# Optimization experiments

Measured on AMD Instinct MI355X. Metric: run time of the kernel, lower is better.

Reference implementation:

```python
import jax, jax.numpy as jnp
import numpy as np

B, S, D_IN, D_OUT = 4, 2048, 1024, 1024

def setup_inputs() -> dict:
    key = jax.random.key(0)
    ks = jax.random.split(key, 6)
    s = 1.0 / np.sqrt(D_IN)
    return {
        "inputs": jax.random.normal(ks[0], (B, S, D_IN), dtype=jnp.float32),
        "Wq": jax.random.normal(ks[1], (D_IN, D_OUT), dtype=jnp.float32) * s,
        "Wk": jax.random.normal(ks[2], (D_IN, D_OUT), dtype=jnp.float32) * s,
        "Wv": jax.random.normal(ks[3], (D_IN, D_OUT), dtype=jnp.float32) * s,
        "Wo": jax.random.normal(ks[4], (D_OUT, D_OUT), dtype=jnp.float32) * (1.0 / np.sqrt(D_OUT)),
        "bo": jax.random.normal(ks[5], (D_OUT,), dtype=jnp.float32) * 0.01,
    }

def reference(inputs, Wq, Wk, Wv, Wo, bo):
    # QKV projections (no bias, matching qkv_bias=False)
    q = inputs @ Wq  # [B,S,D]
    k = inputs @ Wk
    v = inputs @ Wv
    # naive full attention: scores [B,S,S]
    scores = jnp.einsum('bqd,bkd->bqk', q, k) / jnp.sqrt(jnp.asarray(k.shape[-1], q.dtype))
    attn = jax.nn.softmax(scores, axis=-1)
    out = jnp.einsum('bqk,bkd->bqd', attn, v)
    return out @ Wo + bo
```

## Files before the change

kernel.cpp:

```cpp
#include <hip/hip_runtime.h>
#include <hip/hip_bf16.h>
#include <cstdint>

typedef __attribute__((ext_vector_type(8))) __bf16 bf16x8;
typedef __attribute__((ext_vector_type(4))) float  f32x4;

__device__ __forceinline__ unsigned short f2bf(float x) {
    union { float f; unsigned u; } v; v.f = x;
    unsigned r = v.u + 0x7fffu + ((v.u >> 16) & 1u);
    return (unsigned short)(r >> 16);
}
__device__ __forceinline__ unsigned pack2bf(float a, float b) {
    return (unsigned)f2bf(a) | ((unsigned)f2bf(b) << 16);
}

__device__ __forceinline__ void gld_lds16(const unsigned short* g, unsigned short* l) {
    __builtin_amdgcn_global_load_lds(
        (const __attribute__((address_space(1))) unsigned int*)g,
        (__attribute__((address_space(3))) unsigned int*)l,
        16, 0, 0);
}

__global__ void cvt_kernel(const float* __restrict__ in, unsigned short* __restrict__ out, int n4) {
    int i = blockIdx.x * blockDim.x + threadIdx.x;
    if (i < n4) {
        float4 f = ((const float4*)in)[i];
        ushort4 o;
        o.x = f2bf(f.x); o.y = f2bf(f.y); o.z = f2bf(f.z); o.w = f2bf(f.w);
        ((ushort4*)out)[i] = o;
    }
}

__global__ void wpack_kernel(const float* __restrict__ W, unsigned short* __restrict__ out) {
    int tid  = threadIdx.x;
    int lane = tid & 63;
    int chunk = blockIdx.x * 4 + (tid >> 6);
    int nt = chunk >> 5, k32 = chunk & 31;
    int r = lane & 15, q = lane >> 4;
    const float* src = W + (size_t)(k32*32 + q*8) * 1024 + nt*16 + r;
    unsigned o[4];
#pragma unroll
    for (int i = 0; i < 4; i++)
        o[i] = pack2bf(src[(size_t)(2*i) * 1024], src[(size_t)(2*i+1) * 1024]);
    *(uint4*)(out + (size_t)chunk * 512 + lane * 8) = make_uint4(o[0], o[1], o[2], o[3]);
}

__global__ void softmax_kernel(unsigned short* __restrict__ S) {
    const size_t row = blockIdx.x;
    unsigned short* p = S + row * 2048;
    const int tid = threadIdx.x;
    const int wave = tid >> 6, lane = tid & 63;

    uint4 raw = ((const uint4*)p)[tid];
    unsigned u[4] = {raw.x, raw.y, raw.z, raw.w};
    float x[8];
#pragma unroll
    for (int i = 0; i < 4; i++) {
        x[2*i]   = __uint_as_float(u[i] << 16);
        x[2*i+1] = __uint_as_float(u[i] & 0xffff0000u);
    }
    float m = x[0];
#pragma unroll
    for (int i = 1; i < 8; i++) m = fmaxf(m, x[i]);
#pragma unroll
    for (int off = 32; off >= 1; off >>= 1) m = fmaxf(m, __shfl_xor(m, off, 64));
    __shared__ float sm[4], ss[4];
    if (lane == 0) sm[wave] = m;
    __syncthreads();
    m = fmaxf(fmaxf(sm[0], sm[1]), fmaxf(sm[2], sm[3]));

    float e[8], s = 0.f;
#pragma unroll
    for (int i = 0; i < 8; i++) { e[i] = __expf(x[i] - m); s += e[i]; }
#pragma unroll
    for (int off = 32; off >= 1; off >>= 1) s += __shfl_xor(s, off, 64);
    if (lane == 0) ss[wave] = s;
    __syncthreads();
    s = ss[0] + ss[1] + ss[2] + ss[3];
    float inv = 1.0f / s;

    unsigned o[4];
#pragma unroll
    for (int i = 0; i < 4; i++)
        o[i] = pack2bf(e[2*i] * inv, e[2*i+1] * inv);
    ((uint4*)p)[tid] = make_uint4(o[0], o[1], o[2], o[3]);
}

template<int EPI>
__global__ __launch_bounds__(512, 2)
void gemm8p(const unsigned short* __restrict__ A, const unsigned short* __restrict__ Bpk,
            void* __restrict__ C, unsigned short* __restrict__ Ck, unsigned short* __restrict__ Cv,
            int lda, int ldc, int KS, int ns, float scale,
            long long sA, long long sB, long long sC)
{
    __shared__ __align__(16) char smem[131072];

    const int tid  = threadIdx.x;
    const int lane = tid & 63;
    const int wave = tid >> 6;
    const int bz = blockIdx.z;
    A   += (size_t)bz * sA;
    Bpk += (size_t)bz * sB;

    const int gx = gridDim.x;
    int lin = blockIdx.y * gx + blockIdx.x;
    int cpx = (gx * gridDim.y) >> 3;
    int swz = (lin & 7) * cpx + (lin >> 3);
    const int bm = (swz / gx) * 256;
    const int bn = (swz % gx) * 256;

    const int wm = (wave & 1) * 128;
    const int wn = (wave >> 1) * 64;
    const int ln15 = lane & 15;
    const int quad = lane >> 4;
    const int fko = (quad ^ ((ln15 >> 1) & 3)) * 8;

    const int srow = tid >> 2;
    const int scol = ((tid & 3) ^ ((tid >> 3) & 3)) * 8;
    const unsigned short* paU = A + (size_t)(bm + srow) * lda + scol;
    const unsigned short* paL = A + (size_t)(bm + 128 + srow) * lda + scol;
    const unsigned short* pb0 = Bpk + (size_t)((bn >> 4) + (tid >> 6)) * KS * 512 + lane * 8;
    const long long pbstep = (long long)8 * KS * 512;

    f32x4 acc[8][4];
#pragma unroll
    for (int i = 0; i < 8; i++)
#pragma unroll
        for (int j = 0; j < 4; j++) acc[i][j] = (f32x4){0.f, 0.f, 0.f, 0.f};

    auto stageA = [&](int buf, int t, int k) {
        char* d = smem + buf * 32768 + k * 16384 + tid * 16;
        const unsigned short* s = paU + t * 64 + k * 32;
        gld_lds16(s, (unsigned short*)d);
        gld_lds16(paL + t * 64 + k * 32, (unsigned short*)(d + 8192));
    };
    auto stageB = [&](int buf, int t, int k) {
        char* d = smem + 65536 + buf * 32768 + k * 16384 + (tid >> 6) * 1024 + lane * 16;
        const unsigned short* s = pb0 + (size_t)(2 * t + k) * 512;
        gld_lds16(s, (unsigned short*)d);
        gld_lds16(s + pbstep, (unsigned short*)(d + 8192));
    };
    auto dsread = [&](int buf, int k, int mh, bf16x8* af, bf16x8* bfr) {
        const unsigned short* Ar = (const unsigned short*)(smem + buf * 32768 + k * 16384);
        const unsigned short* Br = (const unsigned short*)(smem + 65536 + buf * 32768 + k * 16384);
#pragma unroll
        for (int i = 0; i < 4; i++)
            af[i] = *(const bf16x8*)&Ar[(wm + mh * 64 + i * 16 + ln15) * 32 + fko];
#pragma unroll
        for (int j = 0; j < 4; j++)
            bfr[j] = *(const bf16x8*)&Br[((wn >> 4) + j) * 512 + lane * 8];
    };
    auto mfma16 = [&](int mh, const bf16x8* af, const bf16x8* bfr) {
        __builtin_amdgcn_s_setprio(1);
#pragma unroll
        for (int i = 0; i < 4; i++)
#pragma unroll
            for (int j = 0; j < 4; j++)
                acc[mh * 4 + i][j] = __builtin_amdgcn_mfma_f32_16x16x32_bf16(
                    af[i], bfr[j], acc[mh * 4 + i][j], 0, 0, 0);
        __builtin_amdgcn_s_setprio(0);
    };

#define SB    __builtin_amdgcn_sched_barrier(0)
#define BAR   __builtin_amdgcn_s_barrier()
#define LGKM0 asm volatile("s_waitcnt lgkmcnt(0)" ::: "memory")
#define VM4   asm volatile("s_waitcnt vmcnt(4)" ::: "memory")

    stageB(0, 0, 0); stageA(0, 0, 0); stageB(0, 0, 1); stageA(0, 0, 1); SB;
    VM4; SB; BAR; SB;

    bf16x8 af[4], bfr[4];
    for (int t = 0; t < ns; ++t) {
        const int buf = t & 1, nb = buf ^ 1;
        const int tn = (t + 1 < ns) ? t + 1 : 0;
        dsread(buf, 0, 0, af, bfr); SB; stageB(nb, tn, 0); SB; BAR; SB;
        LGKM0; SB; mfma16(0, af, bfr); SB; BAR; SB;
        dsread(buf, 0, 1, af, bfr); SB; stageA(nb, tn, 0); SB; BAR; SB;
        LGKM0; SB; mfma16(1, af, bfr); SB; VM4; SB; BAR; SB;
        dsread(buf, 1, 0, af, bfr); SB; stageB(nb, tn, 1); SB; BAR; SB;
        LGKM0; SB; mfma16(0, af, bfr); SB; BAR; SB;
        dsread(buf, 1, 1, af, bfr); SB; stageA(nb, tn, 1); SB; BAR; SB;
        LGKM0; SB; mfma16(1, af, bfr); SB; VM4; SB; BAR; SB;
    }
#undef SB
#undef BAR
#undef LGKM0
#undef VM4

    if (EPI == 1) {
        __syncthreads();
        float* ep = (float*)(smem + wave * 4352);
        unsigned short* Co = (unsigned short*)C + (size_t)bz * sC;
#pragma unroll
        for (int i = 0; i < 8; i++) {
#pragma unroll
            for (int j = 0; j < 4; j++)
#pragma unroll
                for (int r = 0; r < 4; r++)
                    ep[(quad*4 + r) * 68 + j*16 + ln15] = acc[i][j][r] * scale;
            __builtin_amdgcn_s_waitcnt(0);
#pragma unroll
            for (int pp = 0; pp < 2; pp++) {
                int lrow = pp*8 + (lane >> 3);
                int col0 = (lane & 7) * 8;
                float4 lo = *(const float4*)&ep[lrow * 68 + col0];
                float4 hi = *(const float4*)&ep[lrow * 68 + col0 + 4];
                uint4 o;
                o.x = pack2bf(lo.x, lo.y); o.y = pack2bf(lo.z, lo.w);
                o.z = pack2bf(hi.x, hi.y); o.w = pack2bf(hi.z, hi.w);
                *(uint4*)&Co[(size_t)(bm + wm + i*16 + lrow) * ldc + bn + wn + col0] = o;
            }
            __builtin_amdgcn_s_waitcnt(0);
        }
    } else {
        __syncthreads();
        float* ep = (float*)(smem + wave * 8704);
        const int region = bn >> 10;
#pragma unroll
        for (int g = 0; g < 4; g++) {
#pragma unroll
            for (int ii = 0; ii < 2; ii++) {
                int i = g*2 + ii;
#pragma unroll
                for (int j = 0; j < 4; j++)
#pragma unroll
                    for (int r = 0; r < 4; r++)
                        ep[(ii*16 + quad*4 + r) * 68 + j*16 + ln15] = acc[i][j][r] * scale;
            }
            __builtin_amdgcn_s_waitcnt(0);
            const int mrow0 = bm + wm + g*32;
            if (region == 0) {
                unsigned short* Q = (unsigned short*)C;
#pragma unroll
                for (int pp = 0; pp < 4; pp++) {
                    int lrow = pp*8 + (lane >> 3);
                    int col0 = (lane & 7) * 8;
                    float4 lo = *(const float4*)&ep[lrow * 68 + col0];
                    float4 hi = *(const float4*)&ep[lrow * 68 + col0 + 4];
                    uint4 o;
                    o.x = pack2bf(lo.x, lo.y); o.y = pack2bf(lo.z, lo.w);
                    o.z = pack2bf(hi.x, hi.y); o.w = pack2bf(hi.z, hi.w);
                    *(uint4*)&Q[(size_t)(mrow0 + lrow) * ldc + bn + wn + col0] = o;
                }
            } else if (region == 1) {
#pragma unroll
                for (int mt = 0; mt < 2; mt++)
#pragma unroll
                    for (int c = 0; c < 2; c++) {
                        float4 f0 = *(const float4*)&ep[(mt*16 + ln15) * 68 + c*32 + quad*8];
                        float4 f1 = *(const float4*)&ep[(mt*16 + ln15) * 68 + c*32 + quad*8 + 4];
                        uint4 o;
                        o.x = pack2bf(f0.x, f0.y); o.y = pack2bf(f0.z, f0.w);
                        o.z = pack2bf(f1.x, f1.y); o.w = pack2bf(f1.z, f1.w);
                        int cid = ((mrow0 + mt*16) >> 4) * 32 + ((bn - 1024 + wn + c*32) >> 5);
                        *(uint4*)(Ck + (size_t)cid * 512 + lane * 8) = o;
                    }
            } else {
                int s32 = mrow0 >> 5;
#pragma unroll
                for (int dt = 0; dt < 4; dt++) {
                    float v[8];
#pragma unroll
                    for (int e = 0; e < 8; e++)
                        v[e] = ep[(quad*8 + e) * 68 + dt*16 + ln15];
                    uint4 o;
                    o.x = pack2bf(v[0], v[1]); o.y = pack2bf(v[2], v[3]);
                    o.z = pack2bf(v[4], v[5]); o.w = pack2bf(v[6], v[7]);
                    int cid = (((bn - 2048 + wn) >> 4) + dt) * 256 + s32;
                    *(uint4*)(Cv + (size_t)cid * 512 + lane * 8) = o;
                }
            }
            __builtin_amdgcn_s_waitcnt(0);
        }
    }
}

template<int EPI>
__global__ __launch_bounds__(512, 2)
void gemm_pk(const unsigned short* __restrict__ A, const unsigned short* __restrict__ Bpk,
             void* __restrict__ C, unsigned short* __restrict__ Ck, unsigned short* __restrict__ Cv,
             const float* __restrict__ bias,
             int lda, int ldc, int KS, int ns, float scale,
             long long sA, long long sB, long long sC)
{
    __shared__ __align__(16) char smem[98304];

    const int tid  = threadIdx.x;
    const int lane = tid & 63;
    const int wave = tid >> 6;
    const int bz = blockIdx.z;
    A   += (size_t)bz * sA;
    Bpk += (size_t)bz * sB;

    const int gx = gridDim.x;
    int lin = blockIdx.y * gx + blockIdx.x;
    int cpx = (gx * gridDim.y) >> 3;
    int swz = (lin & 7) * cpx + (lin >> 3);
    const int bm = (swz / gx) * 256;
    const int bn = (swz % gx) * 128;

    const int srow = tid >> 2;
    const int scol = ((tid & 3) ^ ((tid >> 3) & 3)) * 8;
    const unsigned short* pa0 = A + (size_t)(bm + srow) * lda + scol;
    const unsigned short* pa1 = pa0 + 32;
    const unsigned short* pa2 = A + (size_t)(bm + 128 + srow) * lda + scol;
    const unsigned short* pa3 = pa2 + 32;

    const int wm = (wave & 3) * 64;
    const int wn = (wave >> 2) * 64;
    const int ln15 = lane & 15;
    const int quad = lane >> 4;
    const int fko = (quad ^ ((ln15 >> 1) & 3)) * 8;
    const int rbase = (wm >> 7) * 4096 + (wm & 127) * 32;
    const int ldsoff = tid * 16;

    const unsigned short* pb[4];
#pragma unroll
    for (int j = 0; j < 4; j++)
        pb[j] = Bpk + (size_t)(((bn + wn + j*16) >> 4) * KS) * 512 + lane * 8;

    f32x4 acc[4][4];
#pragma unroll
    for (int i = 0; i < 4; i++)
#pragma unroll
        for (int j = 0; j < 4; j++) acc[i][j] = (f32x4){0.f, 0.f, 0.f, 0.f};

    auto dma = [&](int buf) {
        char* base = smem + buf * 32768;
        gld_lds16(pa0, (unsigned short*)(base + ldsoff));
        gld_lds16(pa2, (unsigned short*)(base + 8192  + ldsoff));
        gld_lds16(pa1, (unsigned short*)(base + 16384 + ldsoff));
        gld_lds16(pa3, (unsigned short*)(base + 24576 + ldsoff));
        pa0 += 64; pa1 += 64; pa2 += 64; pa3 += 64;
    };
    auto loadB = [&](bf16x8* br) {
#pragma unroll
        for (int j = 0; j < 4; j++) {
            br[j]     = *(const bf16x8*)(pb[j]);
            br[4 + j] = *(const bf16x8*)(pb[j] + 512);
            pb[j] += 1024;
        }
    };
    auto phase = [&](const unsigned short* As, int t, const bf16x8* br) {
        bf16x8 af[4];
#pragma unroll
        for (int i = 0; i < 4; i++)
            af[i] = *(const bf16x8*)&As[t*8192 + rbase + i*512 + ln15*32 + fko];
        __builtin_amdgcn_s_setprio(1);
#pragma unroll
        for (int i = 0; i < 4; i++)
#pragma unroll
            for (int j = 0; j < 4; j++)
                acc[i][j] = __builtin_amdgcn_mfma_f32_16x16x32_bf16(
                    af[i], br[t*4 + j], acc[i][j], 0, 0, 0);
        __builtin_amdgcn_s_setprio(0);
    };

#define SB __builtin_amdgcn_sched_barrier(0)
    bf16x8 b0[8], b1[8];
    SB; dma(0); SB; loadB(b0); SB; dma(1); SB;

    int p = 0;
    for (int it = 0; it < ns; it += 2) {
        const unsigned short* As0 = (const unsigned short*)(smem + p * 32768);
        int p1 = p + 1; if (p1 >= 3) p1 -= 3;
        int q0 = p + 2; if (q0 >= 3) q0 -= 3;
        const unsigned short* As1 = (const unsigned short*)(smem + p1 * 32768);
        const bool more = (it + 2 < ns);

        asm volatile("s_waitcnt vmcnt(12)" ::: "memory");
        SB; __builtin_amdgcn_s_barrier(); SB;
        loadB(b1); SB;
        phase(As0, 0, b0);
        __builtin_amdgcn_s_barrier(); SB;
        if (more) { dma(q0); SB; }
        phase(As0, 1, b0);

        if (more) { asm volatile("s_waitcnt vmcnt(12)" ::: "memory"); }
        else      { asm volatile("s_waitcnt vmcnt(8)"  ::: "memory"); }
        SB; __builtin_amdgcn_s_barrier(); SB;
        if (more) { loadB(b0); SB; }
        phase(As1, 0, b1);
        __builtin_amdgcn_s_barrier(); SB;
        if (it + 3 < ns) { dma(p); SB; }
        phase(As1, 1, b1);

        p = q0;
    }
#undef SB

    if (EPI == 0) {
        float bval[4];
#pragma unroll
        for (int j = 0; j < 4; j++) bval[j] = bias[bn + wn + j*16 + ln15];
        float* Co = (float*)C + (size_t)bz * sC;
#pragma unroll
        for (int i = 0; i < 4; i++) {
            int r0 = bm + wm + i*16 + quad*4;
#pragma unroll
            for (int j = 0; j < 4; j++) {
                int c = bn + wn + j*16 + ln15;
#pragma unroll
                for (int r = 0; r < 4; r++)
                    Co[(size_t)(r0 + r) * ldc + c] = acc[i][j][r] * scale + bval[j];
            }
        }
    } else if (EPI == 1) {
        __syncthreads();
        float* ep = (float*)(smem + wave * 4352);
        unsigned short* Co = (unsigned short*)C + (size_t)bz * sC;
#pragma unroll
        for (int i = 0; i < 4; i++) {
#pragma unroll
            for (int j = 0; j < 4; j++)
#pragma unroll
                for (int r = 0; r < 4; r++)
                    ep[(quad*4 + r) * 68 + j*16 + ln15] = acc[i][j][r] * scale;
            __builtin_amdgcn_s_waitcnt(0);
#pragma unroll
            for (int pp = 0; pp < 2; pp++) {
                int lrow = pp*8 + (lane >> 3);
                int col0 = (lane & 7) * 8;
                float4 lo = *(const float4*)&ep[lrow * 68 + col0];
                float4 hi = *(const float4*)&ep[lrow * 68 + col0 + 4];
                uint4 o;
                o.x = pack2bf(lo.x, lo.y); o.y = pack2bf(lo.z, lo.w);
                o.z = pack2bf(hi.x, hi.y); o.w = pack2bf(hi.z, hi.w);
                *(uint4*)&Co[(size_t)(bm + wm + i*16 + lrow) * ldc + bn + wn + col0] = o;
            }
            __builtin_amdgcn_s_waitcnt(0);
        }
    }
}

extern "C" void kernel_launch(void* const* d_in, const int* in_sizes, int n_in,
                              void* d_out, int out_size, void* d_ws, size_t ws_size,
                              hipStream_t stream) {
    const float* X  = (const float*)d_in[0];
    const float* Wq = (const float*)d_in[1];
    const float* Wk = (const float*)d_in[2];
    const float* Wv = (const float*)d_in[3];
    const float* Wo = (const float*)d_in[4];
    const float* bo = (const float*)d_in[5];
    float* out = (float*)d_out;

    size_t off = 0;
    auto alloc = [&](size_t bytes) {
        void* p = (char*)d_ws + off;
        off += (bytes + 255) & ~(size_t)255;
        return p;
    };
    unsigned short* Xbf  = (unsigned short*)alloc(8192ull * 1024 * 2);
    unsigned short* Wpk  = (unsigned short*)alloc(192ull * 32 * 512 * 2);
    unsigned short* Wopk = (unsigned short*)alloc(64ull * 32 * 512 * 2);
    unsigned short* Qrm  = (unsigned short*)alloc(8192ull * 1024 * 2);
    unsigned short* Kpk  = (unsigned short*)alloc(512ull * 32 * 512 * 2);
    unsigned short* Vpk  = (unsigned short*)alloc(64ull * 256 * 512 * 2);
    unsigned short* Sc   = (unsigned short*)alloc(4ull * 2048 * 2048 * 2);
    unsigned short* AO   = Xbf;

    cvt_kernel<<<(8192*1024/4 + 255)/256, 256, 0, stream>>>(X, Xbf, 8192*1024/4);
    wpack_kernel<<<512, 256, 0, stream>>>(Wq, Wpk);
    wpack_kernel<<<512, 256, 0, stream>>>(Wk, Wpk + 64*32*512);
    wpack_kernel<<<512, 256, 0, stream>>>(Wv, Wpk + 128*32*512);
    wpack_kernel<<<512, 256, 0, stream>>>(Wo, Wopk);

    gemm8p<2><<<dim3(3072/256, 8192/256, 1), 512, 0, stream>>>(
        Xbf, Wpk, Qrm, Kpk, Vpk, 1024, 1024, 32, 16, 1.0f, 0, 0, 0);

    gemm8p<1><<<dim3(2048/256, 2048/256, 4), 512, 0, stream>>>(
        Qrm, Kpk, Sc, nullptr, nullptr, 1024, 2048, 32, 16, 0.03125f,
        2048ll*1024, 128ll*32*512, 2048ll*2048);

    softmax_kernel<<<8192, 256, 0, stream>>>(Sc);

    gemm_pk<1><<<dim3(1024/128, 2048/256, 4), 512, 0, stream>>>(
        Sc, Vpk, AO, nullptr, nullptr, nullptr, 2048, 1024, 256, 32, 1.0f,
        2048ll*2048, 64ll*512, 2048ll*1024);

    gemm_pk<0><<<dim3(1024/128, 8192/256, 1), 512, 0, stream>>>(
        AO, Wopk, out, nullptr, nullptr, bo, 1024, 1024, 32, 16, 1.0f, 0, 0, 0);

    (void)n_in; (void)in_sizes; (void)out_size; (void)ws_size;
}
```

Before: 287.3 us.

## Merge GEMM main-loop phases into two larger read/MFMA stages per tile

Each k-tile iteration of the GEMM main loop now runs two phases instead of four. Each phase reads all eight A fragments plus four B fragments from LDS, issues both the A and B global-to-LDS prefetches together, and then runs 32 MFMAs. This halves the number of workgroup barriers and waitcnt points per tile and gives the scheduler longer MFMA runs, which should cut synchronisation overhead. In exchange it holds more fragment registers live, which may reduce occupancy, and it overlaps less LDS and prefetch traffic with compute. Compiler memory fences are added around barriers, and the epilogue indexing is rewritten into an equivalent form.

Result: no change. 281.9 us (-1.9%).

```diff
diff --git a/kernel.cpp b/kernel.cpp
--- a/kernel.cpp
+++ b/kernel.cpp
@@ -140,50 +140,58 @@
         gld_lds16(s, (unsigned short*)d);
         gld_lds16(s + pbstep, (unsigned short*)(d + 8192));
     };
-    auto dsread = [&](int buf, int k, int mh, bf16x8* af, bf16x8* bfr) {
+    auto dsread12 = [&](int buf, int k, bf16x8* af, bf16x8* bfr) {
         const unsigned short* Ar = (const unsigned short*)(smem + buf * 32768 + k * 16384);
         const unsigned short* Br = (const unsigned short*)(smem + 65536 + buf * 32768 + k * 16384);
 #pragma unroll
-        for (int i = 0; i < 4; i++)
-            af[i] = *(const bf16x8*)&Ar[(wm + mh * 64 + i * 16 + ln15) * 32 + fko];
+        for (int im = 0; im < 8; im++)
+            af[im] = *(const bf16x8*)&Ar[(wm + (im >> 2) * 64 + (im & 3) * 16 + ln15) * 32 + fko];
 #pragma unroll
         for (int j = 0; j < 4; j++)
             bfr[j] = *(const bf16x8*)&Br[((wn >> 4) + j) * 512 + lane * 8];
     };
-    auto mfma16 = [&](int mh, const bf16x8* af, const bf16x8* bfr) {
+    auto mfma32 = [&](const bf16x8* af, const bf16x8* bfr) {
         __builtin_amdgcn_s_setprio(1);
 #pragma unroll
-        for (int i = 0; i < 4; i++)
+        for (int im = 0; im < 8; im++)
 #pragma unroll
             for (int j = 0; j < 4; j++)
-                acc[mh * 4 + i][j] = __builtin_amdgcn_mfma_f32_16x16x32_bf16(
-                    af[i], bfr[j], acc[mh * 4 + i][j], 0, 0, 0);
+                acc[im][j] = __builtin_amdgcn_mfma_f32_16x16x32_bf16(
+                    af[im], bfr[j], acc[im][j], 0, 0, 0);
         __builtin_amdgcn_s_setprio(0);
     };
 
 #define SB    __builtin_amdgcn_sched_barrier(0)
 #define BAR   __builtin_amdgcn_s_barrier()
+#define FEN   asm volatile("" ::: "memory")
 #define LGKM0 asm volatile("s_waitcnt lgkmcnt(0)" ::: "memory")
 #define VM4   asm volatile("s_waitcnt vmcnt(4)" ::: "memory")
 
     stageB(0, 0, 0); stageA(0, 0, 0); stageB(0, 0, 1); stageA(0, 0, 1); SB;
-    VM4; SB; BAR; SB;
-
-    bf16x8 af[4], bfr[4];
+    VM4; SB; FEN; BAR; FEN;
+
+    bf16x8 af[8], bfr[4];
     for (int t = 0; t < ns; ++t) {
         const int buf = t & 1, nb = buf ^ 1;
         const int tn = (t + 1 < ns) ? t + 1 : 0;
-        dsread(buf, 0, 0, af, bfr); SB; stageB(nb, tn, 0); SB; BAR; SB;
-        LGKM0; SB; mfma16(0, af, bfr); SB; BAR; SB;
-        dsread(buf, 0, 1, af, bfr); SB; stageA(nb, tn, 0); SB; BAR; SB;
-        LGKM0; SB; mfma16(1, af, bfr); SB; VM4; SB; BAR; SB;
-        dsread(buf, 1, 0, af, bfr); SB; stageB(nb, tn, 1); SB; BAR; SB;
-        LGKM0; SB; mfma16(0, af, bfr); SB; BAR; SB;
-        dsread(buf, 1, 1, af, bfr); SB; stageA(nb, tn, 1); SB; BAR; SB;
-        LGKM0; SB; mfma16(1, af, bfr); SB; VM4; SB; BAR; SB;
+        dsread12(buf, 0, af, bfr); SB;
+        stageB(nb, tn, 0); stageA(nb, tn, 0); SB;
+        FEN; BAR; FEN;
+        LGKM0; SB;
+        mfma32(af, bfr); SB;
+        VM4; SB;
+        FEN; BAR; FEN;
+        dsread12(buf, 1, af, bfr); SB;
+        stageB(nb, tn, 1); stageA(nb, tn, 1); SB;
+        FEN; BAR; FEN;
+        LGKM0; SB;
+        mfma32(af, bfr); SB;
+        VM4; SB;
+        FEN; BAR; FEN;
     }
 #undef SB
 #undef BAR
+#undef FEN
 #undef LGKM0
 #undef VM4
 
@@ -192,12 +200,13 @@
         float* ep = (float*)(smem + wave * 4352);
         unsigned short* Co = (unsigned short*)C + (size_t)bz * sC;
 #pragma unroll
-        for (int i = 0; i < 8; i++) {
+        for (int im = 0; im < 8; im++) {
+            int mrow = (im >> 2) * 64 + (im & 3) * 16;
 #pragma unroll
             for (int j = 0; j < 4; j++)
 #pragma unroll
                 for (int r = 0; r < 4; r++)
-                    ep[(quad*4 + r) * 68 + j*16 + ln15] = acc[i][j][r] * scale;
+                    ep[(quad*4 + r) * 68 + j*16 + ln15] = acc[im][j][r] * scale;
             __builtin_amdgcn_s_waitcnt(0);
 #pragma unroll
             for (int pp = 0; pp < 2; pp++) {
@@ -208,7 +217,7 @@
                 uint4 o;
                 o.x = pack2bf(lo.x, lo.y); o.y = pack2bf(lo.z, lo.w);
                 o.z = pack2bf(hi.x, hi.y); o.w = pack2bf(hi.z, hi.w);
-                *(uint4*)&Co[(size_t)(bm + wm + i*16 + lrow) * ldc + bn + wn + col0] = o;
+                *(uint4*)&Co[(size_t)(bm + wm + mrow + lrow) * ldc + bn + wn + col0] = o;
             }
             __builtin_amdgcn_s_waitcnt(0);
         }
@@ -220,12 +229,12 @@
         for (int g = 0; g < 4; g++) {
 #pragma unroll
             for (int ii = 0; ii < 2; ii++) {
-                int i = g*2 + ii;
+                int im = ((g*2 + ii) >> 2) * 4 + ((g*2 + ii) & 3);
 #pragma unroll
                 for (int j = 0; j < 4; j++)
 #pragma unroll
                     for (int r = 0; r < 4; r++)
-                        ep[(ii*16 + quad*4 + r) * 68 + j*16 + ln15] = acc[i][j][r] * scale;
+                        ep[(ii*16 + quad*4 + r) * 68 + j*16 + ln15] = acc[im][j][r] * scale;
             }
             __builtin_amdgcn_s_waitcnt(0);
             const int mrow0 = bm + wm + g*32;
```
